# Performance work log

Hardware: AMD Instinct MI355X
Metric: run time of the kernel (lower is better)

The kernel has to match this reference:

```python
import jax, jax.numpy as jnp
import numpy as np

HOURS = 24
SU, SL, TU, TL = 100.0, 0.0, 100.0, 0.0
N, M, L, E = 32, 128, 128, 128
T_DIM, U_DIM, L_DIM = 25, 2000, 10000


def setup_inputs() -> dict:
    key = jax.random.key(0)
    ks = jax.random.split(key, 18)
    s = 0.02
    full_seq = jax.random.randint(ks[0], (N, M), 1, L_DIM)
    time_seq = jax.random.randint(ks[1], (N, M), 1, 720)
    user = jax.random.randint(ks[2], (N,), 1, U_DIM)
    posneg = jax.random.randint(ks[3], (N, L), 1, L_DIM)
    traj_len = jax.random.randint(ks[4], (N,), 1, M + 1)
    mat1 = jax.random.uniform(ks[5], (N, M, M, 2), dtype=jnp.float32) * 100.0
    mat2 = jax.random.uniform(ks[6], (N, M, L), dtype=jnp.float32) * 100.0
    vec = jax.random.uniform(ks[7], (N, M), dtype=jnp.float32) * 100.0
    def tab(k, n):  # embedding table with padding_idx=0 zeroed
        return (jax.random.normal(k, (n, E), dtype=jnp.float32) * s).at[0].set(0.0)
    emb_t = tab(ks[8], T_DIM)
    emb_u = tab(ks[9], U_DIM)
    emb_loc = tab(ks[10], L_DIM)
    emb_sl = tab(ks[11], 2)
    emb_su = tab(ks[12], 2)
    emb_tl = tab(ks[13], 2)
    emb_tu = tab(ks[14], 2)
    Wq = jax.random.normal(ks[15], (E, E), dtype=jnp.float32) * s
    Wk = jax.random.normal(ks[16], (E, E), dtype=jnp.float32) * s
    Wv = jax.random.normal(ks[17], (E, E), dtype=jnp.float32) * s
    return dict(full_seq=full_seq, time_seq=time_seq, user=user, posneg=posneg,
                traj_len=traj_len, mat1=mat1, mat2=mat2, vec=vec,
                emb_t=emb_t, emb_u=emb_u, emb_loc=emb_loc,
                emb_sl=emb_sl, emb_su=emb_su, emb_tl=emb_tl, emb_tu=emb_tu,
                Wq=Wq, Wk=Wk, Wv=Wv)


def _interval(e_l, e_u, d, lo, hi):
    # (e_l*(hi-d) + e_u*(d-lo)) / (hi-lo); e_* are [...,E], d is [...]
    return (e_l * (hi - d)[..., None] + e_u * (d - lo)[..., None]) / (hi - lo)


def reference(full_seq, time_seq, user, posneg, traj_len, mat1, mat2, vec,
              emb_t, emb_u, emb_loc, emb_sl, emb_su, emb_tl, emb_tu, Wq, Wk, Wv):
    n, m = full_seq.shape
    tim = (time_seq - 1) % HOURS + 1
    joint = emb_t[tim] + emb_loc[full_seq] + emb_u[user][:, None, :]  # [N,M,E]

    # --- stage 1: self-attention with spatiotemporal relative bias ---
    delta_s, delta_t = mat1[..., 0], mat1[..., 1]  # [N,M,M]
    valid = (jnp.arange(m)[None, :] < traj_len[:, None]).astype(jnp.int32)  # [N,M]
    mask2d = valid[:, None, :] * valid[:, :, None]  # [N,M,M] in {0,1}
    delta = (_interval(emb_sl[mask2d], emb_su[mask2d], delta_s, SL, SU)
             + _interval(emb_tl[mask2d], emb_tu[mask2d], delta_t, TL, TU)).sum(-1)
    fmask = mask2d.astype(joint.dtype)
    q = joint @ Wq.T
    k = joint @ Wk.T
    v = joint @ Wv.T
    attn = jax.nn.softmax(jnp.einsum('bme,bne->bmn', q, k) + delta, axis=-1) * fmask
    self_attn = jnp.einsum('bmn,bne->bme', attn, v)  # [N,M,E]

    # --- stage 2: candidate attention ---
    mask1 = valid[:, :, None]  # [N,M,1]
    sp = _interval(emb_sl[mask1], emb_su[mask1], mat2, SL, SU)            # [N,M,L,E]
    tm = _interval(emb_tl[mask1], emb_tu[mask1], vec[:, :, None], TL, TU)  # [N,M,1,E]
    self_delta = jnp.swapaxes((sp + tm).sum(-1), -1, -2)  # [N,L,M]
    cand = emb_loc[posneg]  # [N,L,E]
    attn2 = jnp.einsum('ble,bme->blm', cand, self_attn) * self_delta
    return attn2.sum(-1)  # [N,L]
```

## Files before the change

### kernel.cpp

```cpp
#include <hip/hip_runtime.h>
#include <hip/hip_bf16.h>

#define HOURS 24
#define NB 32
#define MM 128
#define EE 128

typedef short bf16x8 __attribute__((ext_vector_type(8)));
typedef float f32x4 __attribute__((ext_vector_type(4)));

__device__ __forceinline__ unsigned short f2bfu(float f) {
    __hip_bfloat16 h = __float2bfloat16(f);
    return __builtin_bit_cast(unsigned short, h);
}
__device__ __forceinline__ unsigned int pack2(float a, float b) {
    return (unsigned int)f2bfu(a) | ((unsigned int)f2bfu(b) << 16);
}
__device__ __forceinline__ int swz8(int row, int unit) {
    return row * 128 + (((unit ^ (row & 7)) & 15) << 3);
}
__device__ __forceinline__ bf16x8 load_w_frag(const float* base) {
    float4 x = *(const float4*)base;
    float4 y = *(const float4*)(base + 4);
    union { unsigned int u[4]; bf16x8 v; } r;
    r.u[0] = pack2(x.x, x.y); r.u[1] = pack2(x.z, x.w);
    r.u[2] = pack2(y.x, y.y); r.u[3] = pack2(y.z, y.w);
    return r.v;
}

#define MFMA(a, b, c) __builtin_amdgcn_mfma_f32_16x16x32_bf16(a, b, c, 0, 0, 0)

__global__ __launch_bounds__(256) void k_qkv(
    const int* __restrict__ time_seq, const int* __restrict__ full_seq,
    const int* __restrict__ user,
    const float* __restrict__ emb_t, const float* __restrict__ emb_u,
    const float* __restrict__ emb_loc,
    const float* __restrict__ Wq, const float* __restrict__ Wk, const float* __restrict__ Wv,
    short* __restrict__ qws, short* __restrict__ kws, short* __restrict__ vtws)
{
    __shared__ alignas(16) short Jl[64 * 128];
    int b = blockIdx.y;
    int which = blockIdx.x >> 1;
    int half = blockIdx.x & 1;
    int m0 = half * 64;
    int tid = threadIdx.x;
    int l = tid & 63, w = tid >> 6;
    int lr = l & 15, lg = l >> 4;

    int uid = user[b];
    const float4* Eu4 = (const float4*)(emb_u + (size_t)uid * 128);
#pragma unroll
    for (int it = 0; it < 8; ++it) {
        int i4 = it * 256 + tid;
        int mm = i4 >> 5;
        int fq = i4 & 31;
        int m = m0 + mm;
        int t = time_seq[b * MM + m];
        int tim = (t - 1) % HOURS + 1;
        int loc = full_seq[b * MM + m];
        float4 a = ((const float4*)(emb_t + (size_t)tim * 128))[fq];
        float4 c = ((const float4*)(emb_loc + (size_t)loc * 128))[fq];
        float4 u = Eu4[fq];
        uint2 pk;
        pk.x = pack2(a.x + c.x + u.x, a.y + c.y + u.y);
        pk.y = pack2(a.z + c.z + u.z, a.w + c.w + u.w);
        *(uint2*)&Jl[swz8(mm, fq >> 1) + (fq & 1) * 4] = pk;
    }
    __syncthreads();

    if (which < 2) {
        const float* W = which ? Wk : Wq;
        short* outp = which ? kws : qws;
        bf16x8 af[2][4];
#pragma unroll
        for (int nt = 0; nt < 2; ++nt) {
            int n = (2 * w + nt) * 16 + lr;
#pragma unroll
            for (int kf = 0; kf < 4; ++kf)
                af[nt][kf] = load_w_frag(W + (size_t)n * 128 + kf * 32 + lg * 8);
        }
        f32x4 acc[2][4];
#pragma unroll
        for (int nt = 0; nt < 2; ++nt)
#pragma unroll
            for (int mt = 0; mt < 4; ++mt) acc[nt][mt] = (f32x4){0.f, 0.f, 0.f, 0.f};
#pragma unroll
        for (int mt = 0; mt < 4; ++mt) {
            bf16x8 bf[4];
#pragma unroll
            for (int kf = 0; kf < 4; ++kf)
                bf[kf] = *(const bf16x8*)&Jl[swz8(mt * 16 + lr, kf * 4 + lg)];
#pragma unroll
            for (int nt = 0; nt < 2; ++nt)
#pragma unroll
                for (int kf = 0; kf < 4; ++kf)
                    acc[nt][mt] = MFMA(af[nt][kf], bf[kf], acc[nt][mt]);
        }
#pragma unroll
        for (int nt = 0; nt < 2; ++nt)
#pragma unroll
            for (int mt = 0; mt < 4; ++mt) {
                int mg = m0 + mt * 16 + lr;
                int n0 = (2 * w + nt) * 16 + lg * 4;
                uint2 pk;
                pk.x = pack2(acc[nt][mt][0], acc[nt][mt][1]);
                pk.y = pack2(acc[nt][mt][2], acc[nt][mt][3]);
                *(uint2*)&outp[(size_t)(b * MM + mg) * EE + n0] = pk;
            }
    } else {
        bf16x8 bfr[2][4];
#pragma unroll
        for (int nt = 0; nt < 2; ++nt) {
            int n = (2 * w + nt) * 16 + lr;
#pragma unroll
            for (int kf = 0; kf < 4; ++kf)
                bfr[nt][kf] = load_w_frag(Wv + (size_t)n * 128 + kf * 32 + lg * 8);
        }
        f32x4 acc[4][2];
#pragma unroll
        for (int mt = 0; mt < 4; ++mt)
#pragma unroll
            for (int nt = 0; nt < 2; ++nt) acc[mt][nt] = (f32x4){0.f, 0.f, 0.f, 0.f};
#pragma unroll
        for (int mt = 0; mt < 4; ++mt) {
            bf16x8 af[4];
#pragma unroll
            for (int kf = 0; kf < 4; ++kf)
                af[kf] = *(const bf16x8*)&Jl[swz8(mt * 16 + lr, kf * 4 + lg)];
#pragma unroll
            for (int nt = 0; nt < 2; ++nt)
#pragma unroll
                for (int kf = 0; kf < 4; ++kf)
                    acc[mt][nt] = MFMA(af[kf], bfr[nt][kf], acc[mt][nt]);
        }
#pragma unroll
        for (int mt = 0; mt < 4; ++mt)
#pragma unroll
            for (int nt = 0; nt < 2; ++nt) {
                int ng = (2 * w + nt) * 16 + lr;
                int mp = m0 + mt * 16 + lg * 4;
                uint2 pk;
                pk.x = pack2(acc[mt][nt][0], acc[mt][nt][1]);
                pk.y = pack2(acc[mt][nt][2], acc[mt][nt][3]);
                *(uint2*)&vtws[(size_t)(b * MM + ng) * MM + mp] = pk;
            }
    }
}

__global__ __launch_bounds__(256) void k_attn(
    const short* __restrict__ qws, const short* __restrict__ kws,
    const short* __restrict__ vtws,
    const float* __restrict__ mat1, const int* __restrict__ traj_len,
    const float* __restrict__ esl, const float* __restrict__ esu,
    const float* __restrict__ etl, const float* __restrict__ etu,
    short* __restrict__ saws)
{
    __shared__ alignas(16) float Sf[16 * 132];
    __shared__ alignas(16) short Pl[16 * 128];
    __shared__ float coef[8];

    int b = blockIdx.y;
    int i0 = blockIdx.x * 16;
    int tid = threadIdx.x;
    int l = tid & 63, w = tid >> 6;
    int lr = l & 15, lg = l >> 4;
    int tl = traj_len[b];

    {
        const float* tb[4] = {esl, esu, etl, etu};
#pragma unroll
        for (int s = 0; s < 2; ++s) {
            int c = 2 * w + s;
            const float* t = tb[c >> 1];
            float v = t[(c & 1) * 128 + l] + t[(c & 1) * 128 + 64 + l];
#pragma unroll
            for (int off = 32; off >= 1; off >>= 1) v += __shfl_xor(v, off, 64);
            if (l == 0) coef[c] = v;
        }
    }
    bf16x8 qf[4];
#pragma unroll
    for (int kf = 0; kf < 4; ++kf)
        qf[kf] = *(const bf16x8*)&qws[(size_t)(b * MM + i0 + lr) * EE + kf * 32 + lg * 8];

#pragma unroll
    for (int t2 = 0; t2 < 2; ++t2) {
        int jt = 2 * w + t2;
        f32x4 acc = (f32x4){0.f, 0.f, 0.f, 0.f};
#pragma unroll
        for (int kf = 0; kf < 4; ++kf) {
            bf16x8 bf = *(const bf16x8*)&kws[(size_t)(b * MM + jt * 16 + lr) * EE + kf * 32 + lg * 8];
            acc = MFMA(qf[kf], bf, acc);
        }
#pragma unroll
        for (int r = 0; r < 4; ++r)
            Sf[(lg * 4 + r) * 132 + jt * 16 + lr] = acc[r];
    }
    __syncthreads();

    {
        int r16 = tid >> 4, u = tid & 15;
        int j0 = u * 8;
        int i = i0 + r16;
        int mi = (i < tl) ? 1 : 0;
        float c0_1 = coef[1] + coef[5];
        float c1_1 = (coef[3] - coef[1]) * 0.01f;
        float c2_1 = (coef[7] - coef[5]) * 0.01f;
        float c0_0 = coef[0] + coef[4];
        float c1_0 = (coef[2] - coef[0]) * 0.01f;
        float c2_0 = (coef[6] - coef[4]) * 0.01f;
        const float* sb = &Sf[r16 * 132 + j0];
        float4 s01 = *(const float4*)sb;
        float4 s23 = *(const float4*)(sb + 4);
        float sv[8] = {s01.x, s01.y, s01.z, s01.w, s23.x, s23.y, s23.z, s23.w};
        const float4* m14 = (const float4*)(mat1 + ((size_t)(b * MM + i) * MM + j0) * 2);
        float4 d0 = m14[0], d1 = m14[1], d2 = m14[2], d3 = m14[3];
        float ds[8] = {d0.x, d0.z, d1.x, d1.z, d2.x, d2.z, d3.x, d3.z};
        float dt[8] = {d0.y, d0.w, d1.y, d1.w, d2.y, d2.w, d3.y, d3.w};
        float lgv[8];
        int mk[8];
#pragma unroll
        for (int jj = 0; jj < 8; ++jj) {
            int j = j0 + jj;
            mk[jj] = mi & ((j < tl) ? 1 : 0);
            float cc0 = mk[jj] ? c0_1 : c0_0;
            float cc1 = mk[jj] ? c1_1 : c1_0;
            float cc2 = mk[jj] ? c2_1 : c2_0;
            lgv[jj] = sv[jj] + cc0 + cc1 * ds[jj] + cc2 * dt[jj];
        }
        float mx = lgv[0];
#pragma unroll
        for (int jj = 1; jj < 8; ++jj) mx = fmaxf(mx, lgv[jj]);
#pragma unroll
        for (int off = 8; off >= 1; off >>= 1) mx = fmaxf(mx, __shfl_xor(mx, off, 64));
        float ee[8], sum = 0.f;
#pragma unroll
        for (int jj = 0; jj < 8; ++jj) { ee[jj] = __expf(lgv[jj] - mx); sum += ee[jj]; }
#pragma unroll
        for (int off = 8; off >= 1; off >>= 1) sum += __shfl_xor(sum, off, 64);
        float inv = 1.0f / sum;
        uint4 pk;
        pk.x = pack2(ee[0] * inv * mk[0], ee[1] * inv * mk[1]);
        pk.y = pack2(ee[2] * inv * mk[2], ee[3] * inv * mk[3]);
        pk.z = pack2(ee[4] * inv * mk[4], ee[5] * inv * mk[5]);
        pk.w = pack2(ee[6] * inv * mk[6], ee[7] * inv * mk[7]);
        *(uint4*)&Pl[swz8(r16, u)] = pk;
    }
    __syncthreads();

    bf16x8 bp[4];
#pragma unroll
    for (int kf = 0; kf < 4; ++kf)
        bp[kf] = *(const bf16x8*)&Pl[swz8(lr, kf * 4 + lg)];
#pragma unroll
    for (int t2 = 0; t2 < 2; ++t2) {
        int et = 2 * w + t2;
        f32x4 acc = (f32x4){0.f, 0.f, 0.f, 0.f};
#pragma unroll
        for (int kf = 0; kf < 4; ++kf) {
            bf16x8 af = *(const bf16x8*)&vtws[(size_t)(b * MM + et * 16 + lr) * MM + kf * 32 + lg * 8];
            acc = MFMA(af, bp[kf], acc);
        }
        int ig = i0 + lr;
        int e0 = et * 16 + lg * 4;
        uint2 pk;
        pk.x = pack2(acc[0], acc[1]);
        pk.y = pack2(acc[2], acc[3]);
        *(uint2*)&saws[(size_t)(b * MM + ig) * EE + e0] = pk;
    }
}

__global__ __launch_bounds__(256) void k_final(
    const short* __restrict__ saws, const int* __restrict__ posneg,
    const float* __restrict__ emb_loc, const float* __restrict__ mat2,
    const float* __restrict__ vecg, const int* __restrict__ traj_len,
    const float* __restrict__ esl, const float* __restrict__ esu,
    const float* __restrict__ etl, const float* __restrict__ etu,
    float* __restrict__ outp)
{
    __shared__ float coef[8];
    __shared__ float tms[128], bsv[128];
    __shared__ float PART[4][16];

    int b = blockIdx.y;
    int l0 = blockIdx.x * 16;
    int tid = threadIdx.x;
    int l = tid & 63, w = tid >> 6;
    int lr = l & 15, lg = l >> 4;
    int tl = traj_len[b];

    {
        const float* tb[4] = {esl, esu, etl, etu};
#pragma unroll
        for (int s = 0; s < 2; ++s) {
            int c = 2 * w + s;
            const float* t = tb[c >> 1];
            float v = t[(c & 1) * 128 + l] + t[(c & 1) * 128 + 64 + l];
#pragma unroll
            for (int off = 32; off >= 1; off >>= 1) v += __shfl_xor(v, off, 64);
            if (l == 0) coef[c] = v;
        }
    }
    int p = posneg[b * MM + l0 + lr];
    bf16x8 caf[4];
#pragma unroll
    for (int kf = 0; kf < 4; ++kf)
        caf[kf] = load_w_frag(emb_loc + (size_t)p * 128 + kf * 32 + lg * 8);
    __syncthreads();

    if (tid < 128) {
        int vv = (tid < tl) ? 1 : 0;
        float ssl = vv ? coef[1] : coef[0];
        float ssu = vv ? coef[3] : coef[2];
        float stl = vv ? coef[5] : coef[4];
        float stu = vv ? coef[7] : coef[6];
        tms[tid] = ssl + stl + (stu - stl) * 0.01f * vecg[b * MM + tid];
        bsv[tid] = (ssu - ssl) * 0.01f;
    }
    __syncthreads();

    float vout[4] = {0.f, 0.f, 0.f, 0.f};
#pragma unroll
    for (int t2 = 0; t2 < 2; ++t2) {
        int mt = 2 * w + t2;
        f32x4 acc = (f32x4){0.f, 0.f, 0.f, 0.f};
#pragma unroll
        for (int kf = 0; kf < 4; ++kf) {
            bf16x8 bf = *(const bf16x8*)&saws[(size_t)(b * MM + mt * 16 + lr) * EE + kf * 32 + lg * 8];
            acc = MFMA(caf[kf], bf, acc);
        }
        int mloc = mt * 16 + lr;
        float wt = tms[mloc], wb = bsv[mloc];
        float4 m2 = *(const float4*)&mat2[(size_t)(b * MM + mloc) * MM + l0 + lg * 4];
        vout[0] += acc[0] * (wt + wb * m2.x);
        vout[1] += acc[1] * (wt + wb * m2.y);
        vout[2] += acc[2] * (wt + wb * m2.z);
        vout[3] += acc[3] * (wt + wb * m2.w);
    }
#pragma unroll
    for (int r = 0; r < 4; ++r) {
        float v = vout[r];
        v += __shfl_xor(v, 1, 64);
        v += __shfl_xor(v, 2, 64);
        v += __shfl_xor(v, 4, 64);
        v += __shfl_xor(v, 8, 64);
        if (lr == 0) PART[w][lg * 4 + r] = v;
    }
    __syncthreads();
    if (tid < 16)
        outp[b * MM + l0 + tid] = PART[0][tid] + PART[1][tid] + PART[2][tid] + PART[3][tid];
}

extern "C" void kernel_launch(void* const* d_in, const int* in_sizes, int n_in,
                              void* d_out, int out_size, void* d_ws, size_t ws_size,
                              hipStream_t stream) {
    const int* full_seq = (const int*)d_in[0];
    const int* time_seq = (const int*)d_in[1];
    const int* user     = (const int*)d_in[2];
    const int* posneg   = (const int*)d_in[3];
    const int* traj_len = (const int*)d_in[4];
    const float* mat1   = (const float*)d_in[5];
    const float* mat2   = (const float*)d_in[6];
    const float* vec    = (const float*)d_in[7];
    const float* emb_t  = (const float*)d_in[8];
    const float* emb_u  = (const float*)d_in[9];
    const float* emb_loc= (const float*)d_in[10];
    const float* emb_sl = (const float*)d_in[11];
    const float* emb_su = (const float*)d_in[12];
    const float* emb_tl = (const float*)d_in[13];
    const float* emb_tu = (const float*)d_in[14];
    const float* Wq     = (const float*)d_in[15];
    const float* Wk     = (const float*)d_in[16];
    const float* Wv     = (const float*)d_in[17];

    short* qws  = (short*)d_ws;
    short* kws  = qws + (size_t)NB * MM * EE;
    short* vtws = kws + (size_t)NB * MM * EE;
    short* saws = vtws + (size_t)NB * MM * EE;

    k_qkv<<<dim3(6, 32), 256, 0, stream>>>(time_seq, full_seq, user,
                                           emb_t, emb_u, emb_loc,
                                           Wq, Wk, Wv, qws, kws, vtws);
    k_attn<<<dim3(8, 32), 256, 0, stream>>>(qws, kws, vtws, mat1, traj_len,
                                            emb_sl, emb_su, emb_tl, emb_tu, saws);
    k_final<<<dim3(8, 32), 256, 0, stream>>>(saws, posneg, emb_loc, mat2, vec,
                                             traj_len, emb_sl, emb_su, emb_tl, emb_tu,
                                             (float*)d_out);
}
```

Measured before the change: 25.58 us.

## Fuse attention and candidate scoring into one kernel with atomic output reduction

Merges the attention and final scoring kernels. Each 16-row query chunk keeps its self-attention tile in shared memory and immediately multiplies it against the bf16 candidate embeddings, which are gathered by an extra block in the QKV stage. Partial sums over m are combined across chunks with float atomicAdd into an output zeroed by a memset. This removes one kernel launch and the global round trip of the self-attention tensor, at the cost of atomics, an extra memset, and nondeterministic summation order.

```diff
diff --git a/kernel.cpp b/kernel.cpp
--- a/kernel.cpp
+++ b/kernel.cpp
@@ -30,20 +30,38 @@
 
 #define MFMA(a, b, c) __builtin_amdgcn_mfma_f32_16x16x32_bf16(a, b, c, 0, 0, 0)
 
-__global__ __launch_bounds__(256) void k_qkv(
+__global__ __launch_bounds__(256) void k_stage(
     const int* __restrict__ time_seq, const int* __restrict__ full_seq,
-    const int* __restrict__ user,
+    const int* __restrict__ user, const int* __restrict__ posneg,
     const float* __restrict__ emb_t, const float* __restrict__ emb_u,
     const float* __restrict__ emb_loc,
     const float* __restrict__ Wq, const float* __restrict__ Wk, const float* __restrict__ Wv,
-    short* __restrict__ qws, short* __restrict__ kws, short* __restrict__ vtws)
+    short* __restrict__ qws, short* __restrict__ kws, short* __restrict__ vtws,
+    short* __restrict__ candws)
 {
     __shared__ alignas(16) short Jl[64 * 128];
     int b = blockIdx.y;
-    int which = blockIdx.x >> 1;
-    int half = blockIdx.x & 1;
+    int bx = blockIdx.x;
+    int tid = threadIdx.x;
+
+    if (bx == 6) {
+#pragma unroll
+        for (int it = 0; it < 16; ++it) {
+            int u = it * 256 + tid;
+            int lrow = u >> 5, fq = u & 31;
+            int p = posneg[b * MM + lrow];
+            float4 v = ((const float4*)(emb_loc + (size_t)p * 128))[fq];
+            uint2 pk;
+            pk.x = pack2(v.x, v.y);
+            pk.y = pack2(v.z, v.w);
+            *(uint2*)&candws[((size_t)(b * MM) + lrow) * EE + fq * 4] = pk;
+        }
+        return;
+    }
+
+    int which = bx >> 1;
+    int half = bx & 1;
     int m0 = half * 64;
-    int tid = threadIdx.x;
     int l = tid & 63, w = tid >> 6;
     int lr = l & 15, lg = l >> 4;
 
@@ -147,20 +165,24 @@
     }
 }
 
-__global__ __launch_bounds__(256) void k_attn(
+__global__ __launch_bounds__(256) void k_af(
     const short* __restrict__ qws, const short* __restrict__ kws,
-    const short* __restrict__ vtws,
-    const float* __restrict__ mat1, const int* __restrict__ traj_len,
+    const short* __restrict__ vtws, const short* __restrict__ candws,
+    const float* __restrict__ mat1, const float* __restrict__ mat2,
+    const float* __restrict__ vecg, const int* __restrict__ traj_len,
     const float* __restrict__ esl, const float* __restrict__ esu,
     const float* __restrict__ etl, const float* __restrict__ etu,
-    short* __restrict__ saws)
+    float* __restrict__ outp)
 {
     __shared__ alignas(16) float Sf[16 * 132];
     __shared__ alignas(16) short Pl[16 * 128];
+    __shared__ alignas(16) short SAl[16 * 128];
     __shared__ float coef[8];
+    __shared__ float tms[16], bsv[16];
 
     int b = blockIdx.y;
-    int i0 = blockIdx.x * 16;
+    int chunk = blockIdx.x;
+    int i0 = chunk * 16;
     int tid = threadIdx.x;
     int l = tid & 63, w = tid >> 6;
     int lr = l & 15, lg = l >> 4;
@@ -246,109 +268,70 @@
         pk.w = pack2(ee[6] * inv * mk[6], ee[7] * inv * mk[7]);
         *(uint4*)&Pl[swz8(r16, u)] = pk;
     }
-    __syncthreads();
-
-    bf16x8 bp[4];
-#pragma unroll
-    for (int kf = 0; kf < 4; ++kf)
-        bp[kf] = *(const bf16x8*)&Pl[swz8(lr, kf * 4 + lg)];
-#pragma unroll
-    for (int t2 = 0; t2 < 2; ++t2) {
-        int et = 2 * w + t2;
-        f32x4 acc = (f32x4){0.f, 0.f, 0.f, 0.f};
-#pragma unroll
-        for (int kf = 0; kf < 4; ++kf) {
-            bf16x8 af = *(const bf16x8*)&vtws[(size_t)(b * MM + et * 16 + lr) * MM + kf * 32 + lg * 8];
-            acc = MFMA(af, bp[kf], acc);
-        }
-        int ig = i0 + lr;
-        int e0 = et * 16 + lg * 4;
-        uint2 pk;
-        pk.x = pack2(acc[0], acc[1]);
-        pk.y = pack2(acc[2], acc[3]);
-        *(uint2*)&saws[(size_t)(b * MM + ig) * EE + e0] = pk;
-    }
-}
-
-__global__ __launch_bounds__(256) void k_final(
-    const short* __restrict__ saws, const int* __restrict__ posneg,
-    const float* __restrict__ emb_loc, const float* __restrict__ mat2,
-    const float* __restrict__ vecg, const int* __restrict__ traj_len,
-    const float* __restrict__ esl, const float* __restrict__ esu,
-    const float* __restrict__ etl, const float* __restrict__ etu,
-    float* __restrict__ outp)
-{
-    __shared__ float coef[8];
-    __shared__ float tms[128], bsv[128];
-    __shared__ float PART[4][16];
-
-    int b = blockIdx.y;
-    int l0 = blockIdx.x * 16;
-    int tid = threadIdx.x;
-    int l = tid & 63, w = tid >> 6;
-    int lr = l & 15, lg = l >> 4;
-    int tl = traj_len[b];
-
-    {
-        const float* tb[4] = {esl, esu, etl, etu};
-#pragma unroll
-        for (int s = 0; s < 2; ++s) {
-            int c = 2 * w + s;
-            const float* t = tb[c >> 1];
-            float v = t[(c & 1) * 128 + l] + t[(c & 1) * 128 + 64 + l];
-#pragma unroll
-            for (int off = 32; off >= 1; off >>= 1) v += __shfl_xor(v, off, 64);
-            if (l == 0) coef[c] = v;
-        }
-    }
-    int p = posneg[b * MM + l0 + lr];
-    bf16x8 caf[4];
-#pragma unroll
-    for (int kf = 0; kf < 4; ++kf)
-        caf[kf] = load_w_frag(emb_loc + (size_t)p * 128 + kf * 32 + lg * 8);
-    __syncthreads();
-
-    if (tid < 128) {
-        int vv = (tid < tl) ? 1 : 0;
+    if (tid < 16) {
+        int mg = i0 + tid;
+        int vv = (mg < tl) ? 1 : 0;
         float ssl = vv ? coef[1] : coef[0];
         float ssu = vv ? coef[3] : coef[2];
         float stl = vv ? coef[5] : coef[4];
         float stu = vv ? coef[7] : coef[6];
-        tms[tid] = ssl + stl + (stu - stl) * 0.01f * vecg[b * MM + tid];
+        tms[tid] = ssl + stl + (stu - stl) * 0.01f * vecg[b * MM + mg];
         bsv[tid] = (ssu - ssl) * 0.01f;
     }
     __syncthreads();
 
-    float vout[4] = {0.f, 0.f, 0.f, 0.f};
-#pragma unroll
-    for (int t2 = 0; t2 < 2; ++t2) {
-        int mt = 2 * w + t2;
-        f32x4 acc = (f32x4){0.f, 0.f, 0.f, 0.f};
-#pragma unroll
-        for (int kf = 0; kf < 4; ++kf) {
-            bf16x8 bf = *(const bf16x8*)&saws[(size_t)(b * MM + mt * 16 + lr) * EE + kf * 32 + lg * 8];
-            acc = MFMA(caf[kf], bf, acc);
-        }
-        int mloc = mt * 16 + lr;
-        float wt = tms[mloc], wb = bsv[mloc];
-        float4 m2 = *(const float4*)&mat2[(size_t)(b * MM + mloc) * MM + l0 + lg * 4];
-        vout[0] += acc[0] * (wt + wb * m2.x);
-        vout[1] += acc[1] * (wt + wb * m2.y);
-        vout[2] += acc[2] * (wt + wb * m2.z);
-        vout[3] += acc[3] * (wt + wb * m2.w);
-    }
-#pragma unroll
-    for (int r = 0; r < 4; ++r) {
-        float v = vout[r];
-        v += __shfl_xor(v, 1, 64);
-        v += __shfl_xor(v, 2, 64);
-        v += __shfl_xor(v, 4, 64);
-        v += __shfl_xor(v, 8, 64);
-        if (lr == 0) PART[w][lg * 4 + r] = v;
+    {
+        bf16x8 bp[4];
+#pragma unroll
+        for (int kf = 0; kf < 4; ++kf)
+            bp[kf] = *(const bf16x8*)&Pl[swz8(lr, kf * 4 + lg)];
+#pragma unroll
+        for (int t2 = 0; t2 < 2; ++t2) {
+            int et = 2 * w + t2;
+            f32x4 acc = (f32x4){0.f, 0.f, 0.f, 0.f};
+#pragma unroll
+            for (int kf = 0; kf < 4; ++kf) {
+                bf16x8 af = *(const bf16x8*)&vtws[(size_t)(b * MM + et * 16 + lr) * MM + kf * 32 + lg * 8];
+                acc = MFMA(af, bp[kf], acc);
+            }
+            int e0 = et * 16 + lg * 4;
+            uint2 pk;
+            pk.x = pack2(acc[0], acc[1]);
+            pk.y = pack2(acc[2], acc[3]);
+            *(uint2*)&SAl[swz8(lr, e0 >> 3) + (e0 & 7)] = pk;
+        }
     }
     __syncthreads();
-    if (tid < 16)
-        outp[b * MM + l0 + tid] = PART[0][tid] + PART[1][tid] + PART[2][tid] + PART[3][tid];
+
+    {
+        bf16x8 saf[4];
+#pragma unroll
+        for (int kf = 0; kf < 4; ++kf)
+            saf[kf] = *(const bf16x8*)&SAl[swz8(lr, kf * 4 + lg)];
+#pragma unroll
+        for (int t2 = 0; t2 < 2; ++t2) {
+            int lt = 2 * w + t2;
+            f32x4 acc = (f32x4){0.f, 0.f, 0.f, 0.f};
+#pragma unroll
+            for (int kf = 0; kf < 4; ++kf) {
+                bf16x8 cf = *(const bf16x8*)&candws[(size_t)(b * MM + lt * 16 + lr) * EE + kf * 32 + lg * 8];
+                acc = MFMA(saf[kf], cf, acc);
+            }
+            int lG = lt * 16 + lr;
+            float val = 0.f;
+#pragma unroll
+            for (int r = 0; r < 4; ++r) {
+                int m = lg * 4 + r;
+                int mg = i0 + m;
+                float w2 = tms[m] + bsv[m] * mat2[(size_t)(b * MM + mg) * MM + lG];
+                val += acc[r] * w2;
+            }
+            val += __shfl_xor(val, 16, 64);
+            val += __shfl_xor(val, 32, 64);
+            if (lg == 0)
+                atomicAdd(&outp[b * MM + lG], val);
+        }
+    }
 }
 
 extern "C" void kernel_launch(void* const* d_in, const int* in_sizes, int n_in,
@@ -373,17 +356,16 @@
     const float* Wk     = (const float*)d_in[16];
     const float* Wv     = (const float*)d_in[17];
 
-    short* qws  = (short*)d_ws;
-    short* kws  = qws + (size_t)NB * MM * EE;
-    short* vtws = kws + (size_t)NB * MM * EE;
-    short* saws = vtws + (size_t)NB * MM * EE;
-
-    k_qkv<<<dim3(6, 32), 256, 0, stream>>>(time_seq, full_seq, user,
-                                           emb_t, emb_u, emb_loc,
-                                           Wq, Wk, Wv, qws, kws, vtws);
-    k_attn<<<dim3(8, 32), 256, 0, stream>>>(qws, kws, vtws, mat1, traj_len,
-                                            emb_sl, emb_su, emb_tl, emb_tu, saws);
-    k_final<<<dim3(8, 32), 256, 0, stream>>>(saws, posneg, emb_loc, mat2, vec,
-                                             traj_len, emb_sl, emb_su, emb_tl, emb_tu,
-                                             (float*)d_out);
-}
+    short* qws   = (short*)d_ws;
+    short* kws   = qws + (size_t)NB * MM * EE;
+    short* vtws  = kws + (size_t)NB * MM * EE;
+    short* candws= vtws + (size_t)NB * MM * EE;
+
+    hipMemsetAsync(d_out, 0, (size_t)out_size * sizeof(float), stream);
+    k_stage<<<dim3(7, 32), 256, 0, stream>>>(time_seq, full_seq, user, posneg,
+                                             emb_t, emb_u, emb_loc,
+                                             Wq, Wk, Wv, qws, kws, vtws, candws);
+    k_af<<<dim3(8, 32), 256, 0, stream>>>(qws, kws, vtws, candws, mat1, mat2, vec,
+                                          traj_len, emb_sl, emb_su, emb_tl, emb_tu,
+                                          (float*)d_out);
+}
```

Result: slower. 27.26 us (+6.6%).

## Shrink per-block tiles to raise grid size across all three kernels

Applied to the files above, without the earlier changes.

k_qkv now processes 16 rows per block instead of 64, so the grid grows from 192 to 768 blocks. k_attn and k_final now handle 8 rows per block with 512 threads, one wave per 16-column tile, and the mat1, saws and mat2 loads are issued earlier. The goal is to fill more of the MI355X's compute units and hide memory latency at this small problem size. In exchange, each 16x16 MFMA tile does half-wasted work on 8 rows, and weight fragments are reloaded by more blocks.

```diff
diff --git a/kernel.cpp b/kernel.cpp
--- a/kernel.cpp
+++ b/kernel.cpp
@@ -30,7 +30,7 @@
 
 #define MFMA(a, b, c) __builtin_amdgcn_mfma_f32_16x16x32_bf16(a, b, c, 0, 0, 0)
 
-__global__ __launch_bounds__(256) void k_qkv(
+__global__ __launch_bounds__(256, 3) void k_qkv(
     const int* __restrict__ time_seq, const int* __restrict__ full_seq,
     const int* __restrict__ user,
     const float* __restrict__ emb_t, const float* __restrict__ emb_u,
@@ -38,11 +38,11 @@
     const float* __restrict__ Wq, const float* __restrict__ Wk, const float* __restrict__ Wv,
     short* __restrict__ qws, short* __restrict__ kws, short* __restrict__ vtws)
 {
-    __shared__ alignas(16) short Jl[64 * 128];
+    __shared__ alignas(16) short Jl[16 * 128];
     int b = blockIdx.y;
-    int which = blockIdx.x >> 1;
-    int half = blockIdx.x & 1;
-    int m0 = half * 64;
+    int bx = blockIdx.x;
+    int which = bx >> 3;
+    int m0 = (bx & 7) * 16;
     int tid = threadIdx.x;
     int l = tid & 63, w = tid >> 6;
     int lr = l & 15, lg = l >> 4;
@@ -50,10 +50,9 @@
     int uid = user[b];
     const float4* Eu4 = (const float4*)(emb_u + (size_t)uid * 128);
 #pragma unroll
-    for (int it = 0; it < 8; ++it) {
+    for (int it = 0; it < 2; ++it) {
         int i4 = it * 256 + tid;
-        int mm = i4 >> 5;
-        int fq = i4 & 31;
+        int mm = i4 >> 5, fq = i4 & 31;
         int m = m0 + mm;
         int t = time_seq[b * MM + m];
         int tim = (t - 1) % HOURS + 1;
@@ -71,7 +70,7 @@
     if (which < 2) {
         const float* W = which ? Wk : Wq;
         short* outp = which ? kws : qws;
-        bf16x8 af[2][4];
+        bf16x8 af[2][4], bj[4];
 #pragma unroll
         for (int nt = 0; nt < 2; ++nt) {
             int n = (2 * w + nt) * 16 + lr;
@@ -79,36 +78,28 @@
             for (int kf = 0; kf < 4; ++kf)
                 af[nt][kf] = load_w_frag(W + (size_t)n * 128 + kf * 32 + lg * 8);
         }
-        f32x4 acc[2][4];
+#pragma unroll
+        for (int kf = 0; kf < 4; ++kf)
+            bj[kf] = *(const bf16x8*)&Jl[swz8(lr, kf * 4 + lg)];
+        f32x4 acc[2];
+        acc[0] = (f32x4){0.f, 0.f, 0.f, 0.f};
+        acc[1] = (f32x4){0.f, 0.f, 0.f, 0.f};
 #pragma unroll
         for (int nt = 0; nt < 2; ++nt)
 #pragma unroll
-            for (int mt = 0; mt < 4; ++mt) acc[nt][mt] = (f32x4){0.f, 0.f, 0.f, 0.f};
-#pragma unroll
-        for (int mt = 0; mt < 4; ++mt) {
-            bf16x8 bf[4];
-#pragma unroll
             for (int kf = 0; kf < 4; ++kf)
-                bf[kf] = *(const bf16x8*)&Jl[swz8(mt * 16 + lr, kf * 4 + lg)];
-#pragma unroll
-            for (int nt = 0; nt < 2; ++nt)
-#pragma unroll
-                for (int kf = 0; kf < 4; ++kf)
-                    acc[nt][mt] = MFMA(af[nt][kf], bf[kf], acc[nt][mt]);
-        }
-#pragma unroll
-        for (int nt = 0; nt < 2; ++nt)
-#pragma unroll
-            for (int mt = 0; mt < 4; ++mt) {
-                int mg = m0 + mt * 16 + lr;
-                int n0 = (2 * w + nt) * 16 + lg * 4;
-                uint2 pk;
-                pk.x = pack2(acc[nt][mt][0], acc[nt][mt][1]);
-                pk.y = pack2(acc[nt][mt][2], acc[nt][mt][3]);
-                *(uint2*)&outp[(size_t)(b * MM + mg) * EE + n0] = pk;
-            }
+                acc[nt] = MFMA(af[nt][kf], bj[kf], acc[nt]);
+        int mg = m0 + lr;
+#pragma unroll
+        for (int nt = 0; nt < 2; ++nt) {
+            int n0 = (2 * w + nt) * 16 + lg * 4;
+            uint2 pk;
+            pk.x = pack2(acc[nt][0], acc[nt][1]);
+            pk.y = pack2(acc[nt][2], acc[nt][3]);
+            *(uint2*)&outp[(size_t)(b * MM + mg) * EE + n0] = pk;
+        }
     } else {
-        bf16x8 bfr[2][4];
+        bf16x8 bfr[2][4], aj[4];
 #pragma unroll
         for (int nt = 0; nt < 2; ++nt) {
             int n = (2 * w + nt) * 16 + lr;
@@ -116,38 +107,30 @@
             for (int kf = 0; kf < 4; ++kf)
                 bfr[nt][kf] = load_w_frag(Wv + (size_t)n * 128 + kf * 32 + lg * 8);
         }
-        f32x4 acc[4][2];
-#pragma unroll
-        for (int mt = 0; mt < 4; ++mt)
-#pragma unroll
-            for (int nt = 0; nt < 2; ++nt) acc[mt][nt] = (f32x4){0.f, 0.f, 0.f, 0.f};
-#pragma unroll
-        for (int mt = 0; mt < 4; ++mt) {
-            bf16x8 af[4];
+#pragma unroll
+        for (int kf = 0; kf < 4; ++kf)
+            aj[kf] = *(const bf16x8*)&Jl[swz8(lr, kf * 4 + lg)];
+        f32x4 acc[2];
+        acc[0] = (f32x4){0.f, 0.f, 0.f, 0.f};
+        acc[1] = (f32x4){0.f, 0.f, 0.f, 0.f};
+#pragma unroll
+        for (int nt = 0; nt < 2; ++nt)
 #pragma unroll
             for (int kf = 0; kf < 4; ++kf)
-                af[kf] = *(const bf16x8*)&Jl[swz8(mt * 16 + lr, kf * 4 + lg)];
-#pragma unroll
-            for (int nt = 0; nt < 2; ++nt)
-#pragma unroll
-                for (int kf = 0; kf < 4; ++kf)
-                    acc[mt][nt] = MFMA(af[kf], bfr[nt][kf], acc[mt][nt]);
-        }
-#pragma unroll
-        for (int mt = 0; mt < 4; ++mt)
-#pragma unroll
-            for (int nt = 0; nt < 2; ++nt) {
-                int ng = (2 * w + nt) * 16 + lr;
-                int mp = m0 + mt * 16 + lg * 4;
-                uint2 pk;
-                pk.x = pack2(acc[mt][nt][0], acc[mt][nt][1]);
-                pk.y = pack2(acc[mt][nt][2], acc[mt][nt][3]);
-                *(uint2*)&vtws[(size_t)(b * MM + ng) * MM + mp] = pk;
-            }
-    }
-}
-
-__global__ __launch_bounds__(256) void k_attn(
+                acc[nt] = MFMA(aj[kf], bfr[nt][kf], acc[nt]);
+#pragma unroll
+        for (int nt = 0; nt < 2; ++nt) {
+            int ng = (2 * w + nt) * 16 + lr;
+            int mp = m0 + lg * 4;
+            uint2 pk;
+            pk.x = pack2(acc[nt][0], acc[nt][1]);
+            pk.y = pack2(acc[nt][2], acc[nt][3]);
+            *(uint2*)&vtws[(size_t)(b * MM + ng) * MM + mp] = pk;
+        }
+    }
+}
+
+__global__ __launch_bounds__(512, 4) void k_attn(
     const short* __restrict__ qws, const short* __restrict__ kws,
     const short* __restrict__ vtws,
     const float* __restrict__ mat1, const int* __restrict__ traj_len,
@@ -155,122 +138,98 @@
     const float* __restrict__ etl, const float* __restrict__ etu,
     short* __restrict__ saws)
 {
-    __shared__ alignas(16) float Sf[16 * 132];
+    __shared__ alignas(16) float Sf[8 * 132];
     __shared__ alignas(16) short Pl[16 * 128];
     __shared__ float coef[8];
 
     int b = blockIdx.y;
-    int i0 = blockIdx.x * 16;
+    int i0 = blockIdx.x * 8;
     int tid = threadIdx.x;
     int l = tid & 63, w = tid >> 6;
     int lr = l & 15, lg = l >> 4;
     int tl = traj_len[b];
-
-    {
-        const float* tb[4] = {esl, esu, etl, etu};
-#pragma unroll
-        for (int s = 0; s < 2; ++s) {
-            int c = 2 * w + s;
-            const float* t = tb[c >> 1];
-            float v = t[(c & 1) * 128 + l] + t[(c & 1) * 128 + 64 + l];
-#pragma unroll
-            for (int off = 32; off >= 1; off >>= 1) v += __shfl_xor(v, off, 64);
-            if (l == 0) coef[c] = v;
-        }
-    }
-    bf16x8 qf[4];
-#pragma unroll
-    for (int kf = 0; kf < 4; ++kf)
-        qf[kf] = *(const bf16x8*)&qws[(size_t)(b * MM + i0 + lr) * EE + kf * 32 + lg * 8];
-
-#pragma unroll
-    for (int t2 = 0; t2 < 2; ++t2) {
-        int jt = 2 * w + t2;
+    int irow = i0 + w;
+
+    float4 md = *(const float4*)&mat1[((size_t)(b * MM + irow) * MM + 2 * l) * 2];
+
+    if (tid < 512) ((unsigned int*)Pl)[512 + tid] = 0u;
+
+    {
+        const float* tb4[4] = {esl, esu, etl, etu};
+        const float* t = tb4[w >> 1];
+        int row = w & 1;
+        float v = t[row * 128 + l] + t[row * 128 + 64 + l];
+#pragma unroll
+        for (int off = 32; off >= 1; off >>= 1) v += __shfl_xor(v, off, 64);
+        if (l == 0) coef[w] = v;
+    }
+
+    {
+        bf16x8 qf[4], bk[4];
+#pragma unroll
+        for (int kf = 0; kf < 4; ++kf) {
+            qf[kf] = *(const bf16x8*)&qws[(size_t)(b * MM + i0 + (lr & 7)) * EE + kf * 32 + lg * 8];
+            bk[kf] = *(const bf16x8*)&kws[(size_t)(b * MM + w * 16 + lr) * EE + kf * 32 + lg * 8];
+        }
         f32x4 acc = (f32x4){0.f, 0.f, 0.f, 0.f};
 #pragma unroll
-        for (int kf = 0; kf < 4; ++kf) {
-            bf16x8 bf = *(const bf16x8*)&kws[(size_t)(b * MM + jt * 16 + lr) * EE + kf * 32 + lg * 8];
-            acc = MFMA(qf[kf], bf, acc);
-        }
-#pragma unroll
-        for (int r = 0; r < 4; ++r)
-            Sf[(lg * 4 + r) * 132 + jt * 16 + lr] = acc[r];
-    }
-    __syncthreads();
-
-    {
-        int r16 = tid >> 4, u = tid & 15;
-        int j0 = u * 8;
-        int i = i0 + r16;
-        int mi = (i < tl) ? 1 : 0;
+        for (int kf = 0; kf < 4; ++kf) acc = MFMA(qf[kf], bk[kf], acc);
+        if (lg < 2) {
+#pragma unroll
+            for (int r = 0; r < 4; ++r)
+                Sf[(lg * 4 + r) * 132 + w * 16 + lr] = acc[r];
+        }
+    }
+    __syncthreads();
+
+    {
+        float2 sv = *(const float2*)&Sf[w * 132 + 2 * l];
+        int mi = (irow < tl) ? 1 : 0;
         float c0_1 = coef[1] + coef[5];
         float c1_1 = (coef[3] - coef[1]) * 0.01f;
         float c2_1 = (coef[7] - coef[5]) * 0.01f;
         float c0_0 = coef[0] + coef[4];
         float c1_0 = (coef[2] - coef[0]) * 0.01f;
         float c2_0 = (coef[6] - coef[4]) * 0.01f;
-        const float* sb = &Sf[r16 * 132 + j0];
-        float4 s01 = *(const float4*)sb;
-        float4 s23 = *(const float4*)(sb + 4);
-        float sv[8] = {s01.x, s01.y, s01.z, s01.w, s23.x, s23.y, s23.z, s23.w};
-        const float4* m14 = (const float4*)(mat1 + ((size_t)(b * MM + i) * MM + j0) * 2);
-        float4 d0 = m14[0], d1 = m14[1], d2 = m14[2], d3 = m14[3];
-        float ds[8] = {d0.x, d0.z, d1.x, d1.z, d2.x, d2.z, d3.x, d3.z};
-        float dt[8] = {d0.y, d0.w, d1.y, d1.w, d2.y, d2.w, d3.y, d3.w};
-        float lgv[8];
-        int mk[8];
-#pragma unroll
-        for (int jj = 0; jj < 8; ++jj) {
-            int j = j0 + jj;
-            mk[jj] = mi & ((j < tl) ? 1 : 0);
-            float cc0 = mk[jj] ? c0_1 : c0_0;
-            float cc1 = mk[jj] ? c1_1 : c1_0;
-            float cc2 = mk[jj] ? c2_1 : c2_0;
-            lgv[jj] = sv[jj] + cc0 + cc1 * ds[jj] + cc2 * dt[jj];
-        }
-        float mx = lgv[0];
-#pragma unroll
-        for (int jj = 1; jj < 8; ++jj) mx = fmaxf(mx, lgv[jj]);
-#pragma unroll
-        for (int off = 8; off >= 1; off >>= 1) mx = fmaxf(mx, __shfl_xor(mx, off, 64));
-        float ee[8], sum = 0.f;
-#pragma unroll
-        for (int jj = 0; jj < 8; ++jj) { ee[jj] = __expf(lgv[jj] - mx); sum += ee[jj]; }
-#pragma unroll
-        for (int off = 8; off >= 1; off >>= 1) sum += __shfl_xor(sum, off, 64);
+        int mk0 = mi & ((2 * l) < tl ? 1 : 0);
+        int mk1 = mi & ((2 * l + 1) < tl ? 1 : 0);
+        float lg0 = sv.x + (mk0 ? c0_1 : c0_0) + (mk0 ? c1_1 : c1_0) * md.x + (mk0 ? c2_1 : c2_0) * md.y;
+        float lg1 = sv.y + (mk1 ? c0_1 : c0_0) + (mk1 ? c1_1 : c1_0) * md.z + (mk1 ? c2_1 : c2_0) * md.w;
+        float mx = fmaxf(lg0, lg1);
+#pragma unroll
+        for (int off = 32; off >= 1; off >>= 1) mx = fmaxf(mx, __shfl_xor(mx, off, 64));
+        float e0 = __expf(lg0 - mx), e1 = __expf(lg1 - mx);
+        float sum = e0 + e1;
+#pragma unroll
+        for (int off = 32; off >= 1; off >>= 1) sum += __shfl_xor(sum, off, 64);
         float inv = 1.0f / sum;
-        uint4 pk;
-        pk.x = pack2(ee[0] * inv * mk[0], ee[1] * inv * mk[1]);
-        pk.y = pack2(ee[2] * inv * mk[2], ee[3] * inv * mk[3]);
-        pk.z = pack2(ee[4] * inv * mk[4], ee[5] * inv * mk[5]);
-        pk.w = pack2(ee[6] * inv * mk[6], ee[7] * inv * mk[7]);
-        *(uint4*)&Pl[swz8(r16, u)] = pk;
-    }
-    __syncthreads();
-
-    bf16x8 bp[4];
-#pragma unroll
-    for (int kf = 0; kf < 4; ++kf)
-        bp[kf] = *(const bf16x8*)&Pl[swz8(lr, kf * 4 + lg)];
-#pragma unroll
-    for (int t2 = 0; t2 < 2; ++t2) {
-        int et = 2 * w + t2;
+        *(unsigned int*)&Pl[swz8(w, l >> 2) + ((2 * l) & 7)] =
+            pack2(e0 * inv * (float)mk0, e1 * inv * (float)mk1);
+    }
+    __syncthreads();
+
+    {
+        bf16x8 af[4], bp[4];
+#pragma unroll
+        for (int kf = 0; kf < 4; ++kf) {
+            bp[kf] = *(const bf16x8*)&Pl[swz8(lr, kf * 4 + lg)];
+            af[kf] = *(const bf16x8*)&vtws[(size_t)(b * MM + w * 16 + lr) * MM + kf * 32 + lg * 8];
+        }
         f32x4 acc = (f32x4){0.f, 0.f, 0.f, 0.f};
 #pragma unroll
-        for (int kf = 0; kf < 4; ++kf) {
-            bf16x8 af = *(const bf16x8*)&vtws[(size_t)(b * MM + et * 16 + lr) * MM + kf * 32 + lg * 8];
-            acc = MFMA(af, bp[kf], acc);
-        }
-        int ig = i0 + lr;
-        int e0 = et * 16 + lg * 4;
-        uint2 pk;
-        pk.x = pack2(acc[0], acc[1]);
-        pk.y = pack2(acc[2], acc[3]);
-        *(uint2*)&saws[(size_t)(b * MM + ig) * EE + e0] = pk;
-    }
-}
-
-__global__ __launch_bounds__(256) void k_final(
+        for (int kf = 0; kf < 4; ++kf) acc = MFMA(af[kf], bp[kf], acc);
+        if (lr < 8) {
+            int ig = i0 + lr;
+            int e0 = w * 16 + lg * 4;
+            uint2 pk;
+            pk.x = pack2(acc[0], acc[1]);
+            pk.y = pack2(acc[2], acc[3]);
+            *(uint2*)&saws[(size_t)(b * MM + ig) * EE + e0] = pk;
+        }
+    }
+}
+
+__global__ __launch_bounds__(512, 4) void k_final(
     const short* __restrict__ saws, const int* __restrict__ posneg,
     const float* __restrict__ emb_loc, const float* __restrict__ mat2,
     const float* __restrict__ vecg, const int* __restrict__ traj_len,
@@ -278,36 +237,39 @@
     const float* __restrict__ etl, const float* __restrict__ etu,
     float* __restrict__ outp)
 {
-    __shared__ float coef[8];
-    __shared__ float tms[128], bsv[128];
-    __shared__ float PART[4][16];
+    __shared__ float coef[8], tms[128], bsv[128];
+    __shared__ float PART[8][8];
 
     int b = blockIdx.y;
-    int l0 = blockIdx.x * 16;
+    int l0 = blockIdx.x * 8;
     int tid = threadIdx.x;
     int l = tid & 63, w = tid >> 6;
     int lr = l & 15, lg = l >> 4;
     int tl = traj_len[b];
 
-    {
-        const float* tb[4] = {esl, esu, etl, etu};
-#pragma unroll
-        for (int s = 0; s < 2; ++s) {
-            int c = 2 * w + s;
-            const float* t = tb[c >> 1];
-            float v = t[(c & 1) * 128 + l] + t[(c & 1) * 128 + 64 + l];
-#pragma unroll
-            for (int off = 32; off >= 1; off >>= 1) v += __shfl_xor(v, off, 64);
-            if (l == 0) coef[c] = v;
-        }
-    }
-    int p = posneg[b * MM + l0 + lr];
+    int p = posneg[b * MM + l0 + (lr & 7)];
     bf16x8 caf[4];
 #pragma unroll
     for (int kf = 0; kf < 4; ++kf)
         caf[kf] = load_w_frag(emb_loc + (size_t)p * 128 + kf * 32 + lg * 8);
-    __syncthreads();
-
+    float4 m2 = (float4){0.f, 0.f, 0.f, 0.f};
+    if (lg < 2)
+        m2 = *(const float4*)&mat2[(size_t)(b * MM + w * 16 + lr) * MM + l0 + lg * 4];
+    bf16x8 bsa[4];
+#pragma unroll
+    for (int kf = 0; kf < 4; ++kf)
+        bsa[kf] = *(const bf16x8*)&saws[(size_t)(b * MM + w * 16 + lr) * EE + kf * 32 + lg * 8];
+
+    {
+        const float* tb4[4] = {esl, esu, etl, etu};
+        const float* t = tb4[w >> 1];
+        int row = w & 1;
+        float v = t[row * 128 + l] + t[row * 128 + 64 + l];
+#pragma unroll
+        for (int off = 32; off >= 1; off >>= 1) v += __shfl_xor(v, off, 64);
+        if (l == 0) coef[w] = v;
+    }
+    __syncthreads();
     if (tid < 128) {
         int vv = (tid < tl) ? 1 : 0;
         float ssl = vv ? coef[1] : coef[0];
@@ -319,36 +281,32 @@
     }
     __syncthreads();
 
-    float vout[4] = {0.f, 0.f, 0.f, 0.f};
-#pragma unroll
-    for (int t2 = 0; t2 < 2; ++t2) {
-        int mt = 2 * w + t2;
-        f32x4 acc = (f32x4){0.f, 0.f, 0.f, 0.f};
-#pragma unroll
-        for (int kf = 0; kf < 4; ++kf) {
-            bf16x8 bf = *(const bf16x8*)&saws[(size_t)(b * MM + mt * 16 + lr) * EE + kf * 32 + lg * 8];
-            acc = MFMA(caf[kf], bf, acc);
-        }
-        int mloc = mt * 16 + lr;
-        float wt = tms[mloc], wb = bsv[mloc];
-        float4 m2 = *(const float4*)&mat2[(size_t)(b * MM + mloc) * MM + l0 + lg * 4];
-        vout[0] += acc[0] * (wt + wb * m2.x);
-        vout[1] += acc[1] * (wt + wb * m2.y);
-        vout[2] += acc[2] * (wt + wb * m2.z);
-        vout[3] += acc[3] * (wt + wb * m2.w);
-    }
+    f32x4 acc = (f32x4){0.f, 0.f, 0.f, 0.f};
+#pragma unroll
+    for (int kf = 0; kf < 4; ++kf) acc = MFMA(caf[kf], bsa[kf], acc);
+    int m = w * 16 + lr;
+    float wt = tms[m], wb = bsv[m];
+    float val[4];
+    val[0] = acc[0] * (wt + wb * m2.x);
+    val[1] = acc[1] * (wt + wb * m2.y);
+    val[2] = acc[2] * (wt + wb * m2.z);
+    val[3] = acc[3] * (wt + wb * m2.w);
 #pragma unroll
     for (int r = 0; r < 4; ++r) {
-        float v = vout[r];
+        float v = val[r];
         v += __shfl_xor(v, 1, 64);
         v += __shfl_xor(v, 2, 64);
         v += __shfl_xor(v, 4, 64);
         v += __shfl_xor(v, 8, 64);
-        if (lr == 0) PART[w][lg * 4 + r] = v;
-    }
-    __syncthreads();
-    if (tid < 16)
-        outp[b * MM + l0 + tid] = PART[0][tid] + PART[1][tid] + PART[2][tid] + PART[3][tid];
+        if (lr == 0 && lg < 2) PART[w][lg * 4 + r] = v;
+    }
+    __syncthreads();
+    if (tid < 8) {
+        float s = 0.f;
+#pragma unroll
+        for (int w8 = 0; w8 < 8; ++w8) s += PART[w8][tid];
+        outp[b * MM + l0 + tid] = s;
+    }
 }
 
 extern "C" void kernel_launch(void* const* d_in, const int* in_sizes, int n_in,
@@ -378,12 +336,12 @@
     short* vtws = kws + (size_t)NB * MM * EE;
     short* saws = vtws + (size_t)NB * MM * EE;
 
-    k_qkv<<<dim3(6, 32), 256, 0, stream>>>(time_seq, full_seq, user,
-                                           emb_t, emb_u, emb_loc,
-                                           Wq, Wk, Wv, qws, kws, vtws);
-    k_attn<<<dim3(8, 32), 256, 0, stream>>>(qws, kws, vtws, mat1, traj_len,
-                                            emb_sl, emb_su, emb_tl, emb_tu, saws);
-    k_final<<<dim3(8, 32), 256, 0, stream>>>(saws, posneg, emb_loc, mat2, vec,
-                                             traj_len, emb_sl, emb_su, emb_tl, emb_tu,
-                                             (float*)d_out);
-}
+    k_qkv<<<dim3(24, 32), 256, 0, stream>>>(time_seq, full_seq, user,
+                                            emb_t, emb_u, emb_loc,
+                                            Wq, Wk, Wv, qws, kws, vtws);
+    k_attn<<<dim3(16, 32), 512, 0, stream>>>(qws, kws, vtws, mat1, traj_len,
+                                             emb_sl, emb_su, emb_tl, emb_tu, saws);
+    k_final<<<dim3(16, 32), 512, 0, stream>>>(saws, posneg, emb_loc, mat2, vec,
+                                              traj_len, emb_sl, emb_su, emb_tl, emb_tu,
+                                              (float*)d_out);
+}
```

Result: slower. 33.20 us (+29.8%).
